# Kernel optimization log

Measured on AMD Instinct MI355X. Metric: run time of the kernel, lower is better.

Reference implementation:

```python
import jax, jax.numpy as jnp
import numpy as np

INPUT_SIZE = 500
SENTENCE_SIZE = 128


def setup_inputs() -> dict:
    key = jax.random.key(0)
    ks = jax.random.split(key, 20)
    B, D = 16, 512
    Ho, Hi, Hu = 4, 4, 4
    dh_ori = D // Ho          # 128
    dh = D // (Hi + Hu)       # 64
    s = 0.05
    code = jax.random.normal(ks[0], (B, INPUT_SIZE, D), jnp.float32)
    # binary sentence-membership mask (which code tokens belong to each sentence)
    input_sentence = (jax.random.uniform(ks[1], (B, SENTENCE_SIZE, INPUT_SIZE)) < 0.2).astype(jnp.float32)

    def W(k, h, dout):
        return jax.random.normal(k, (h, D, dout), jnp.float32) * s

    def b(k, h, dout):
        return jax.random.normal(k, (h, dout), jnp.float32) * 0.01

    return dict(
        code=code, input_sentence=input_sentence,
        Wq_ori=W(ks[2], Ho, dh_ori), bq_ori=b(ks[3], Ho, dh_ori),
        Wk_ori=W(ks[4], Ho, dh_ori), bk_ori=b(ks[5], Ho, dh_ori),
        Wq_in=W(ks[6], Hi, dh), bq_in=b(ks[7], Hi, dh),
        Wk_in=W(ks[8], Hi, dh), bk_in=b(ks[9], Hi, dh),
        Wv_in=W(ks[10], Hi, dh), bv_in=b(ks[11], Hi, dh),
        Wq_out=W(ks[12], Hu, dh), bq_out=b(ks[13], Hu, dh),
        Wk_out=W(ks[14], Hu, dh), bk_out=b(ks[15], Hu, dh),
        Wv_out=W(ks[16], Hu, dh), bv_out=b(ks[17], Hu, dh),
    )


def _proj(x, W, b):
    # x: (B, N, D), W: (H, D, F), b: (H, F) -> (B, H, N, F), relu Dense per head
    return jax.nn.relu(jnp.einsum('bnd,hdf->bhnf', x, W) + b[:, None, :])


def reference(code, input_sentence,
              Wq_ori, bq_ori, Wk_ori, bk_ori,
              Wq_in, bq_in, Wk_in, bk_in, Wv_in, bv_in,
              Wq_out, bq_out, Wk_out, bk_out, Wv_out, bv_out):
    B, S = input_sentence.shape[0], input_sentence.shape[1]
    sent = input_sentence

    # ---- original (ori) branch: max over heads of raw QK^T, mask, matmul code ----
    q = _proj(code, Wq_ori, bq_ori)
    k = _proj(code, Wk_ori, bk_ori)
    scores_ori = jnp.einsum('bhnf,bhmf->bhnm', q, k).max(axis=1)      # (B, N, N)
    sA = jnp.einsum('bsn,bnm->bsm', sent, scores_ori)                 # (B, S, N)
    out_ori = jnp.einsum('bsm,bmd->bsd', sent * sA, code)             # (B, S, D)

    # ---- in-mask heads ----
    qi = _proj(code, Wq_in, bq_in)
    ki = _proj(code, Wk_in, bk_in)
    vi = _proj(code, Wv_in, bv_in)
    sc = jnp.einsum('bhnf,bhmf->bhnm', qi, ki)                        # (B, Hi, N, N)
    sAi = jnp.einsum('bsn,bhnm->bhsm', sent, sc)                      # (B, Hi, S, N)
    out_in = jnp.einsum('bhsm,bhmf->bhsf', sent[:, None] * sAi, vi)   # (B, Hi, S, F)

    # ---- out-mask heads ----
    qo = _proj(code, Wq_out, bq_out)
    ko = _proj(code, Wk_out, bk_out)
    vo = _proj(code, Wv_out, bv_out)
    sco = jnp.einsum('bhnf,bhmf->bhnm', qo, ko)
    sAo = jnp.einsum('bsn,bhnm->bhsm', sent, sco)
    masked = (sent - 1.0)[:, None] * sAo                              # (B, Hu, S, N)
    include = sent.sum(axis=2)[:, None, :, None]                      # (B, 1, S, 1)
    masked = masked / (INPUT_SIZE - include) * include
    out_out = jnp.einsum('bhsm,bhmf->bhsf', masked, vo)               # (B, Hu, S, F)

    # original returns a list [ori, in_0..in_Hi-1, out_0..out_Hu-1]; concat along features
    in_flat = jnp.transpose(out_in, (0, 2, 1, 3)).reshape(B, S, -1)
    out_flat = jnp.transpose(out_out, (0, 2, 1, 3)).reshape(B, S, -1)
    return jnp.concatenate([out_ori, in_flat, out_flat], axis=-1)
```

## Files before the change

kernel.cpp:

```cpp
#include <hip/hip_runtime.h>
#include <cfloat>

#define B_  16
#define N_  500
#define NP  512
#define S_  128
#define D_  512
#define FO  128
#define FI  64

typedef unsigned short u16;
typedef __attribute__((ext_vector_type(8))) short bf8;
typedef __attribute__((ext_vector_type(4))) float f4;

#define MFMA(a,b,c) __builtin_amdgcn_mfma_f32_16x16x32_bf16((a),(b),(c),0,0,0)

__device__ __forceinline__ u16 f2b(float x){
    union{float f;unsigned u;} v; v.f=x;
    unsigned r = v.u + 0x7fffu + ((v.u>>16)&1u);
    return (u16)(r>>16);
}
__device__ __forceinline__ float b2f(u16 x){
    union{unsigned u;float f;} v; v.u=((unsigned)x)<<16; return v.f;
}
__device__ __forceinline__ bf8 ldb8(const u16* p){ return *(const bf8*)p; }

__device__ __forceinline__ void gl2lds16(const u16* g, u16* lds){
    __builtin_amdgcn_global_load_lds(
        (const __attribute__((address_space(1))) unsigned int*)g,
        (__attribute__((address_space(3))) unsigned int*)lds, 16, 0, 0);
}
__device__ __forceinline__ void vdrain(){
    asm volatile("s_waitcnt vmcnt(0)" ::: "memory");
}

struct PWAll { const float* W[8]; u16* WT[8]; };
__global__ __launch_bounds__(256) void prep_all(const float* __restrict__ code,
                                                u16* __restrict__ codeB,
                                                u16* __restrict__ codeT,
                                                PWAll a)
{
    __shared__ float T[64][65];
    const int t = threadIdx.x;
    const int x = blockIdx.x;
    if (x < 1024){
        const int b  = x >> 6;
        const int m0 = ((x >> 3) & 7) * 64;
        const int d0 = (x & 7) * 64;
        #pragma unroll
        for (int i=0;i<16;++i){
            int idx = t + i*256; int rr = idx>>6, cc = idx&63;
            int m = m0+rr;
            T[rr][cc] = (m < N_) ? code[((size_t)b*N_+m)*D_ + d0+cc] : 0.f;
        }
        __syncthreads();
        #pragma unroll
        for (int i=0;i<16;++i){
            int idx=t+i*256; int rr=idx>>6, cc=idx&63; int m=m0+rr;
            if (m<N_) codeB[((size_t)b*N_+m)*D_ + d0+cc] = f2b(T[rr][cc]);
        }
        #pragma unroll
        for (int i=0;i<16;++i){
            int idx=t+i*256; int dd=idx>>6, mm=idx&63;
            codeT[((size_t)b*D_ + d0+dd)*NP + m0+mm] = f2b(T[mm][dd]);
        }
    } else {
        const int v    = x - 1024;
        const int h    = v / 80;
        const int rem  = v - h*80;
        const int slot = rem >> 3;
        const int d0   = (rem & 7) * 64;
        const int widx = slot<4 ? (slot>>1) : slot-2;
        const int ftile= slot<4 ? (slot&1)  : 0;
        const int F    = slot<4 ? 128 : 64;
        const float* W = a.W[widx];
        u16* WT        = a.WT[widx];
        const int f0 = ftile*64;
        #pragma unroll
        for (int i=0;i<16;++i){
            int idx=t+i*256; int rr=idx>>6, cc=idx&63;
            T[rr][cc] = W[((size_t)h*D_ + d0+rr)*F + f0+cc];
        }
        __syncthreads();
        #pragma unroll
        for (int i=0;i<16;++i){
            int idx=t+i*256; int ff=idx>>6, dd=idx&63;
            WT[((size_t)h*F + f0+ff)*D_ + d0+dd] = f2b(T[dd][ff]);
        }
    }
}

__global__ __launch_bounds__(256) void prep_sent_pad(const float* __restrict__ sent,
                                                     u16* __restrict__ sentB,
                                                     float* __restrict__ inc,
                                                     u16* a0, u16* a1, u16* a2, u16* a3)
{
    const int t = threadIdx.x;
    const int x = blockIdx.x;
    if (x < 1024){
        const int b  = x >> 6;
        const int s  = (x & 63)*2 + (t >> 7);
        const int tl = t & 127;
        const float* row = sent + ((size_t)b*S_+s)*N_;
        float4 v = make_float4(0.f,0.f,0.f,0.f);
        const int n = tl*4;
        if (n < N_) v = *(const float4*)(row+n);
        float sum = v.x+v.y+v.z+v.w;
        ushort4 o; o.x=f2b(v.x); o.y=f2b(v.y); o.z=f2b(v.z); o.w=f2b(v.w);
        *(ushort4*)&sentB[((size_t)b*S_+s)*NP + n] = o;
        #pragma unroll
        for (int off=32; off; off>>=1) sum += __shfl_down(sum, off);
        __shared__ float ls[4];
        if ((t&63)==0) ls[t>>6]=sum;
        __syncthreads();
        if (tl==0) inc[b*S_+s] = ls[(t>>7)*2] + ls[(t>>7)*2+1];
    } else {
        const int u  = x - 1024;
        u16* arr4[4] = {a0,a1,a2,a3};
        u16* base = arr4[u>>6] + (size_t)(u&63)*FI*NP;
        for (int idx=t; idx<FI*12; idx+=256){
            int f = idx/12, n = N_ + idx%12;
            base[(size_t)f*NP + n] = 0;
        }
    }
}

struct GemmOut { const float* bias[8]; u16* dst[8]; };
union ProjLDS {
    u16 ab[4][4096];
    u16 ot[16896];
};
__global__ __launch_bounds__(256) void proj_gemm(const u16* __restrict__ codeB,
                                                 const u16* __restrict__ WallT,
                                                 GemmOut go)
{
    __shared__ alignas(16) ProjLDS L;

    const int t = threadIdx.x;
    const int w = t>>6, l = t&63, lane16 = l&15, lq = l>>4;
    const int bid = blockIdx.x;
    const int xcd = bid & 7;
    const int g   = bid >> 3;
    const int rt  = xcd*8 + g/20;
    const int ct  = g - (g/20)*20;
    const int r0 = rt*128;
    const int c0 = ct*128;
    const int wr = (w>>1)*64, wc = (w&1)*64;
    const int srow = l>>2;

    f4 acc[4][4] = {};

    auto STAGE = [&](u16* Ad, u16* Bd, int k0){
        #pragma unroll
        for (int iss=0; iss<2; ++iss){
            const int rbase = w*32 + iss*16;
            const int R  = rbase + srow;
            const int cg = ((l&3) ^ ((R>>1)&3))*8;
            gl2lds16(codeB + (size_t)(r0+R)*D_ + k0 + cg, Ad + rbase*32);
            gl2lds16(WallT + (size_t)(c0+R)*D_ + k0 + cg, Bd + rbase*32);
        }
    };
    auto COMPUTE = [&](const u16* Ad, const u16* Bd){
        bf8 af[4], bfr[4];
        #pragma unroll
        for (int i=0;i<4;++i){
            const int Ra = wr + i*16 + lane16;
            const int Rb = wc + i*16 + lane16;
            af[i]  = *(const bf8*)&Ad[Ra*32 + ((lq ^ ((Ra>>1)&3))*8)];
            bfr[i] = *(const bf8*)&Bd[Rb*32 + ((lq ^ ((Rb>>1)&3))*8)];
        }
        #pragma unroll
        for (int i=0;i<4;++i)
            #pragma unroll
            for (int j=0;j<4;++j)
                acc[i][j] = MFMA(af[i], bfr[j], acc[i][j]);
    };

    STAGE(L.ab[0], L.ab[2], 0);
    #pragma unroll
    for (int k0=0; k0<D_; k0+=64){
        vdrain(); __syncthreads();
        if (k0+32 < D_) STAGE(L.ab[1], L.ab[3], k0+32);
        COMPUTE(L.ab[0], L.ab[2]);
        vdrain(); __syncthreads();
        if (k0+64 < D_) STAGE(L.ab[0], L.ab[2], k0+64);
        COMPUTE(L.ab[1], L.ab[3]);
    }

    const int ri = (ct<4) ? 0 : (ct<8) ? 1 : 2 + ((ct-8)>>1);
    const bool tr = (ri==2)||(ri==4)||(ri==5)||(ri==7);

    vdrain(); __syncthreads();

    #pragma unroll
    for (int j=0;j<4;++j){
        const int c = c0 + wc + j*16 + lane16;
        const int idx = (c < 1024) ? (c & 511) : ((c-1024) & 255);
        const float bv = go.bias[ri][idx];
        if (tr){
            #pragma unroll
            for (int i=0;i<4;++i){
                ushort4 o4;
                float x0=acc[i][j][0]+bv, x1=acc[i][j][1]+bv, x2=acc[i][j][2]+bv, x3=acc[i][j][3]+bv;
                o4.x=f2b(x0>0.f?x0:0.f); o4.y=f2b(x1>0.f?x1:0.f);
                o4.z=f2b(x2>0.f?x2:0.f); o4.w=f2b(x3>0.f?x3:0.f);
                *(ushort4*)&L.ot[(wc+j*16+lane16)*132 + wr+i*16+lq*4] = o4;
            }
        } else {
            #pragma unroll
            for (int i=0;i<4;++i)
                #pragma unroll
                for (int reg=0;reg<4;++reg){
                    float x = acc[i][j][reg] + bv;
                    L.ot[(wr+i*16+lq*4+reg)*132 + wc+j*16+lane16] = f2b(x>0.f?x:0.f);
                }
        }
    }
    __syncthreads();

    if (tr){
        const int c  = t>>1;
        const int cg = c0 + c;
        const int u  = cg - 1024;
        const int hfv = u & 255, h = hfv>>6, f2 = hfv & 63;
        u16* dbase = go.dst[ri];
        const int half = t & 1;
        #pragma unroll
        for (int k2=0;k2<16;++k2){
            const int r  = half*64 + k2*4;
            const int rb = r0 + r;
            if (rb < 8000){
                const int b = rb/500, n = rb - b*500;
                *(ushort4*)&dbase[((size_t)(b*4+h)*FI + f2)*NP + n] =
                    *(const ushort4*)&L.ot[c*132 + r];
            }
        }
    } else {
        const int r  = t>>1;
        const int rb = r0 + r;
        if (rb < 8000){
            const int b = rb/500, n = rb - b*500;
            const int half = t & 1;
            const int cg0 = c0 + half*64;
            int h, f2base, F2;
            if (cg0 < 1024){ const int hf0 = cg0 & 511; h = hf0>>7; f2base = hf0 & 127; F2 = 128; }
            else           { const int hf0 = (cg0-1024) & 255; h = hf0>>6; f2base = hf0 & 63; F2 = 64; }
            u16* dstp = go.dst[ri] + ((size_t)(b*4+h)*N_ + n)*F2 + f2base;
            #pragma unroll
            for (int k2=0;k2<16;++k2)
                *(ushort4*)&dstp[k2*4] = *(const ushort4*)&L.ot[r*132 + half*64 + k2*4];
        }
    }
}

__global__ __launch_bounds__(256) void ms_mfma(const u16* __restrict__ q,
                                               const u16* __restrict__ k,
                                               u16* __restrict__ maxscT)
{
    __shared__ alignas(16) u16 Qs[64][136];
    __shared__ alignas(16) u16 Ks[128][136];
    const int t=threadIdx.x, w=t>>6, l=t&63, lane16=l&15, lq=l>>4;
    const int b=blockIdx.x, n0=blockIdx.y*64, m0=blockIdx.z*128;
    const int wr=(w>>1)*32, wc=(w&1)*64;

    f4 best[2][4];
    #pragma unroll
    for(int rt=0;rt<2;++rt)
        #pragma unroll
        for(int ct=0;ct<4;++ct)
            #pragma unroll
            for(int i=0;i<4;++i) best[rt][ct][i] = -FLT_MAX;

    for (int h=0;h<4;++h){
        const u16* qh = q + (size_t)(b*4+h)*N_*FO;
        const u16* kh = k + (size_t)(b*4+h)*N_*FO;
        #pragma unroll
        for (int i=0;i<4;++i){
            const int e=t+i*256, row=e>>4, kc=(e&15)*8;
            int n=n0+row; if(n>N_-1)n=N_-1;
            *(bf8*)&Qs[row][kc] = ldb8(qh + (size_t)n*FO + kc);
        }
        #pragma unroll
        for (int i=0;i<8;++i){
            const int e=t+i*256, row=e>>4, kc=(e&15)*8;
            int m=m0+row; if(m>N_-1)m=N_-1;
            *(bf8*)&Ks[row][kc] = ldb8(kh + (size_t)m*FO + kc);
        }
        __syncthreads();
        f4 acc[2][4]={};
        #pragma unroll
        for (int kk=0;kk<FO;kk+=32){
            bf8 a0=*(const bf8*)&Qs[wr+lane16][kk+lq*8];
            bf8 a1=*(const bf8*)&Qs[wr+16+lane16][kk+lq*8];
            #pragma unroll
            for(int ct=0;ct<4;++ct){
                bf8 bb=*(const bf8*)&Ks[wc+ct*16+lane16][kk+lq*8];
                acc[0][ct]=MFMA(a0,bb,acc[0][ct]);
                acc[1][ct]=MFMA(a1,bb,acc[1][ct]);
            }
        }
        #pragma unroll
        for(int rt=0;rt<2;++rt)
            #pragma unroll
            for(int ct=0;ct<4;++ct)
                #pragma unroll
                for(int i=0;i<4;++i) best[rt][ct][i] = fmaxf(best[rt][ct][i], acc[rt][ct][i]);
        __syncthreads();
    }
    #pragma unroll
    for(int rt=0;rt<2;++rt)
        #pragma unroll
        for(int ct=0;ct<4;++ct){
            const int m  = m0+wc+ct*16+lane16;
            const int nb = n0+wr+rt*16+lq*4;
            ushort4 o; o.x=f2b(best[rt][ct][0]); o.y=f2b(best[rt][ct][1]);
            o.z=f2b(best[rt][ct][2]); o.w=f2b(best[rt][ct][3]);
            *(ushort4*)&maxscT[((size_t)b*NP+m)*NP + nb] = o;
        }
}

__global__ __launch_bounds__(512) void saoo(const u16* __restrict__ sentB,
                                            const u16* __restrict__ maxscT,
                                            const u16* __restrict__ codeT,
                                            float* __restrict__ out)
{
    __shared__ u16 sAmS[16][520];
    const int b=blockIdx.x, s0=blockIdx.y*16;
    const int t=threadIdx.x, w=t>>6, l=t&63, lane16=l&15, lq=l>>4;

    {
        const int m0 = w*64;
        const u16* ap = sentB + ((size_t)b*S_ + s0+lane16)*NP + lq*8;
        const u16* bp[4];
        #pragma unroll
        for(int ct=0;ct<4;++ct) bp[ct] = maxscT + ((size_t)b*NP + m0+ct*16+lane16)*NP + lq*8;
        f4 acc[4] = {};
        for (int k0=0;k0<NP;k0+=32){
            bf8 av=ldb8(ap+k0);
            #pragma unroll
            for(int ct=0;ct<4;++ct) acc[ct]=MFMA(av, ldb8(bp[ct]+k0), acc[ct]);
        }
        #pragma unroll
        for(int ct=0;ct<4;++ct){
            const int m = m0+ct*16+lane16;
            #pragma unroll
            for(int reg=0;reg<4;++reg){
                const int s = s0+lq*4+reg;
                const float sv = b2f(sentB[((size_t)b*S_+s)*NP+m]);
                sAmS[lq*4+reg][m] = (sv != 0.f) ? f2b(acc[ct][reg]*sv) : (u16)0;
            }
        }
    }
    __syncthreads();
    {
        const int d0 = w*64;
        const u16* bp[4];
        #pragma unroll
        for(int ct=0;ct<4;++ct) bp[ct] = codeT + ((size_t)b*D_ + d0+ct*16+lane16)*NP + lq*8;
        f4 acc[4] = {};
        for (int k0=0;k0<NP;k0+=32){
            bf8 av = *(const bf8*)&sAmS[lane16][k0+lq*8];
            #pragma unroll
            for(int ct=0;ct<4;++ct) acc[ct]=MFMA(av, ldb8(bp[ct]+k0), acc[ct]);
        }
        #pragma unroll
        for(int ct=0;ct<4;++ct){
            const int d = d0+ct*16+lane16;
            #pragma unroll
            for(int reg=0;reg<4;++reg){
                const int s = s0+lq*4+reg;
                out[((size_t)b*S_+s)*1024 + d] = acc[ct][reg];
            }
        }
    }
}

struct AttnArgs { const u16* qT[2]; const u16* kp[2]; const u16* vT[2]; };
__global__ __launch_bounds__(256) void attn_fused(AttnArgs a,
                                                  const u16* __restrict__ sentB,
                                                  const float* __restrict__ inc,
                                                  float* __restrict__ out)
{
    __shared__ float red[4][32][68];
    __shared__ u16 qsS[32][72];
    __shared__ u16 Pw[4][32][72];
    const int bh=blockIdx.x, b=bh>>2, h=bh&3, s0=blockIdx.y*32, br=blockIdx.z;
    const u16* qT = a.qT[br];
    const u16* kp = a.kp[br];
    const u16* vT = a.vT[br];
    const int t=threadIdx.x, w=t>>6, l=t&63, lane16=l&15, lq=l>>4;

    {
        const u16 *ap[2], *bp[4];
        #pragma unroll
        for(int rt=0;rt<2;++rt) ap[rt] = sentB + ((size_t)b*S_ + s0+rt*16+lane16)*NP + w*128 + lq*8;
        #pragma unroll
        for(int ct=0;ct<4;++ct) bp[ct] = qT + ((size_t)bh*FI + ct*16+lane16)*NP + w*128 + lq*8;
        f4 acc[2][4] = {};
        #pragma unroll
        for (int k0=0;k0<128;k0+=32){
            bf8 a0=ldb8(ap[0]+k0), a1=ldb8(ap[1]+k0);
            #pragma unroll
            for(int ct=0;ct<4;++ct){
                bf8 bb=ldb8(bp[ct]+k0);
                acc[0][ct]=MFMA(a0,bb,acc[0][ct]);
                acc[1][ct]=MFMA(a1,bb,acc[1][ct]);
            }
        }
        #pragma unroll
        for(int rt=0;rt<2;++rt)
            #pragma unroll
            for(int ct=0;ct<4;++ct)
                #pragma unroll
                for(int reg=0;reg<4;++reg)
                    red[w][rt*16+lq*4+reg][ct*16+lane16] = acc[rt][ct][reg];
    }
    __syncthreads();
    {
        const int s=t>>3, f0=(t&7)*8;
        #pragma unroll
        for (int j=0;j<8;++j){
            float v = red[0][s][f0+j]+red[1][s][f0+j]+red[2][s][f0+j]+red[3][s][f0+j];
            qsS[s][f0+j] = f2b(v);
        }
    }
    __syncthreads();

    f4 accO[2][4] = {};
    #pragma unroll
    for (int c=0;c<2;++c){
        const int m0 = w*64 + c*256;
        f4 p[2][4] = {};
        const u16* bp[4];
        #pragma unroll
        for(int ct=0;ct<4;++ct){
            int m=m0+ct*16+lane16; if(m>N_-1)m=N_-1;
            bp[ct] = kp + ((size_t)bh*N_+m)*FI + lq*8;
        }
        #pragma unroll
        for (int kk=0; kk<FI; kk+=32){
            bf8 a0 = *(const bf8*)&qsS[lane16][kk+lq*8];
            bf8 a1 = *(const bf8*)&qsS[16+lane16][kk+lq*8];
            #pragma unroll
            for(int ct=0;ct<4;++ct){
                bf8 bb=ldb8(bp[ct]+kk);
                p[0][ct]=MFMA(a0,bb,p[0][ct]);
                p[1][ct]=MFMA(a1,bb,p[1][ct]);
            }
        }
        #pragma unroll
        for(int rt=0;rt<2;++rt)
            #pragma unroll
            for(int ct=0;ct<4;++ct){
                const int m = m0+ct*16+lane16;
                #pragma unroll
                for(int reg=0;reg<4;++reg){
                    const int s = s0+rt*16+lq*4+reg;
                    const float sv = b2f(sentB[((size_t)b*S_+s)*NP+m]);
                    const float wgt = br ? ((m<N_)? sv-1.f : 0.f) : sv;
                    Pw[w][rt*16+lq*4+reg][ct*16+lane16] = f2b(p[rt][ct][reg]*wgt);
                }
            }
        #pragma unroll
        for (int kk2=0; kk2<64; kk2+=32){
            bf8 a2[2];
            #pragma unroll
            for(int rt=0;rt<2;++rt) a2[rt] = *(const bf8*)&Pw[w][rt*16+lane16][kk2+lq*8];
            #pragma unroll
            for(int ct=0;ct<4;++ct){
                bf8 vv = ldb8(vT + ((size_t)bh*FI + ct*16+lane16)*NP + m0+kk2+lq*8);
                accO[0][ct]=MFMA(a2[0],vv,accO[0][ct]);
                accO[1][ct]=MFMA(a2[1],vv,accO[1][ct]);
            }
        }
    }
    #pragma unroll
    for(int rt=0;rt<2;++rt)
        #pragma unroll
        for(int ct=0;ct<4;++ct)
            #pragma unroll
            for(int reg=0;reg<4;++reg)
                red[w][rt*16+lq*4+reg][ct*16+lane16] = accO[rt][ct][reg];
    __syncthreads();
    {
        const int s=t>>3, f0=(t&7)*8;
        float fac = 1.f;
        if (br){ const float ic = inc[b*S_+s0+s]; fac = ic/(500.f-ic); }
        const size_t o = ((size_t)b*S_+s0+s)*1024 + (br?768:512) + h*FI + f0;
        #pragma unroll
        for (int j=0;j<8;++j){
            float v = red[0][s][f0+j]+red[1][s][f0+j]+red[2][s][f0+j]+red[3][s][f0+j];
            out[o+j] = v*fac;
        }
    }
}

extern "C" void kernel_launch(void* const* d_in, const int* in_sizes, int n_in,
                              void* d_out, int out_size, void* d_ws, size_t ws_size,
                              hipStream_t stream)
{
    const float* code   = (const float*)d_in[0];
    const float* sent   = (const float*)d_in[1];
    const float* Wq_ori = (const float*)d_in[2];
    const float* bq_ori = (const float*)d_in[3];
    const float* Wk_ori = (const float*)d_in[4];
    const float* bk_ori = (const float*)d_in[5];
    const float* Wq_in  = (const float*)d_in[6];
    const float* bq_in  = (const float*)d_in[7];
    const float* Wk_in  = (const float*)d_in[8];
    const float* bk_in  = (const float*)d_in[9];
    const float* Wv_in  = (const float*)d_in[10];
    const float* bv_in  = (const float*)d_in[11];
    const float* Wq_out = (const float*)d_in[12];
    const float* bq_out = (const float*)d_in[13];
    const float* Wk_out = (const float*)d_in[14];
    const float* bk_out = (const float*)d_in[15];
    const float* Wv_out = (const float*)d_in[16];
    const float* bv_out = (const float*)d_in[17];
    float* out = (float*)d_out;

    char* w = (char*)d_ws;
    u16*   codeB  = (u16*)(w);
    u16*   WallT  = (u16*)(w + 8388608);
    u16*   WTqo   = WallT;
    u16*   WTko   = WallT +  262144;
    u16*   WTqi   = WallT +  524288;
    u16*   WTki   = WallT +  655360;
    u16*   WTvi   = WallT +  786432;
    u16*   WTqu   = WallT +  917504;
    u16*   WTku   = WallT + 1048576;
    u16*   WTvu   = WallT + 1179648;
    u16*   sentB  = (u16*)(w + 11010048);
    float* incp   = (float*)(w + 13107200);
    u16* q_ori  = (u16*)(w + 13115392);
    u16* k_ori  = (u16*)(w + 21307392);
    u16* maxscT = (u16*)(w + 29499392);
    u16* codeT  = (u16*)(w + 37888000);
    u16* k_in   = (u16*)(w + 46276608);
    u16* k_out  = (u16*)(w + 50372608);
    u16* qT_in  = (u16*)(w + 54468608);
    u16* qT_out = (u16*)(w + 58662912);
    u16* vT_in  = (u16*)(w + 62857216);
    u16* vT_out = (u16*)(w + 67051520);

    PWAll pw;
    pw.W[0]=Wq_ori; pw.W[1]=Wk_ori; pw.W[2]=Wq_in; pw.W[3]=Wk_in;
    pw.W[4]=Wv_in;  pw.W[5]=Wq_out; pw.W[6]=Wk_out; pw.W[7]=Wv_out;
    pw.WT[0]=WTqo; pw.WT[1]=WTko; pw.WT[2]=WTqi; pw.WT[3]=WTki;
    pw.WT[4]=WTvi; pw.WT[5]=WTqu; pw.WT[6]=WTku; pw.WT[7]=WTvu;
    prep_all<<<dim3(1344), 256, 0, stream>>>(code, codeB, codeT, pw);
    prep_sent_pad<<<dim3(1280), 256, 0, stream>>>(sent, sentB, incp,
                                                  qT_in, qT_out, vT_in, vT_out);

    GemmOut go;
    go.bias[0]=bq_ori; go.bias[1]=bk_ori; go.bias[2]=bq_in; go.bias[3]=bk_in;
    go.bias[4]=bv_in;  go.bias[5]=bq_out; go.bias[6]=bk_out; go.bias[7]=bv_out;
    go.dst[0]=q_ori; go.dst[1]=k_ori; go.dst[2]=qT_in; go.dst[3]=k_in;
    go.dst[4]=vT_in; go.dst[5]=qT_out; go.dst[6]=k_out; go.dst[7]=vT_out;
    proj_gemm<<<dim3(1280), 256, 0, stream>>>(codeB, WallT, go);

    ms_mfma<<<dim3(16,8,4), 256, 0, stream>>>(q_ori, k_ori, maxscT);
    saoo<<<dim3(16,8), 512, 0, stream>>>(sentB, maxscT, codeT, out);

    AttnArgs aa;
    aa.qT[0]=qT_in;  aa.qT[1]=qT_out;
    aa.kp[0]=k_in;   aa.kp[1]=k_out;
    aa.vT[0]=vT_in;  aa.vT[1]=vT_out;
    attn_fused<<<dim3(64,4,2), 256, 0, stream>>>(aa, sentB, incp, out);
}
```

Measured before the change: 133.1 us.

## Merge prep kernels and co-schedule max-score with attention in one launch

```diff
diff --git a/kernel.cpp b/kernel.cpp
--- a/kernel.cpp
+++ b/kernel.cpp
@@ -35,10 +35,14 @@
 }
 
 struct PWAll { const float* W[8]; u16* WT[8]; };
-__global__ __launch_bounds__(256) void prep_all(const float* __restrict__ code,
-                                                u16* __restrict__ codeB,
-                                                u16* __restrict__ codeT,
-                                                PWAll a)
+__global__ __launch_bounds__(256) void prep_fused(const float* __restrict__ code,
+                                                  u16* __restrict__ codeB,
+                                                  u16* __restrict__ codeT,
+                                                  PWAll a,
+                                                  const float* __restrict__ sent,
+                                                  u16* __restrict__ sentB,
+                                                  float* __restrict__ inc,
+                                                  u16* a0, u16* a1, u16* a2, u16* a3)
 {
     __shared__ float T[64][65];
     const int t = threadIdx.x;
@@ -64,7 +68,7 @@
             int idx=t+i*256; int dd=idx>>6, mm=idx&63;
             codeT[((size_t)b*D_ + d0+dd)*NP + m0+mm] = f2b(T[mm][dd]);
         }
-    } else {
+    } else if (x < 1344){
         const int v    = x - 1024;
         const int h    = v / 80;
         const int rem  = v - h*80;
@@ -87,19 +91,10 @@
             int idx=t+i*256; int ff=idx>>6, dd=idx&63;
             WT[((size_t)h*F + f0+ff)*D_ + d0+dd] = f2b(T[dd][ff]);
         }
-    }
-}
-
-__global__ __launch_bounds__(256) void prep_sent_pad(const float* __restrict__ sent,
-                                                     u16* __restrict__ sentB,
-                                                     float* __restrict__ inc,
-                                                     u16* a0, u16* a1, u16* a2, u16* a3)
-{
-    const int t = threadIdx.x;
-    const int x = blockIdx.x;
-    if (x < 1024){
-        const int b  = x >> 6;
-        const int s  = (x & 63)*2 + (t >> 7);
+    } else if (x < 2368){
+        const int y  = x - 1344;
+        const int b  = y >> 6;
+        const int s  = (y & 63)*2 + (t >> 7);
         const int tl = t & 127;
         const float* row = sent + ((size_t)b*S_+s)*N_;
         float4 v = make_float4(0.f,0.f,0.f,0.f);
@@ -115,7 +110,7 @@
         __syncthreads();
         if (tl==0) inc[b*S_+s] = ls[(t>>7)*2] + ls[(t>>7)*2+1];
     } else {
-        const int u  = x - 1024;
+        const int u  = x - 2368;
         u16* arr4[4] = {a0,a1,a2,a3};
         u16* base = arr4[u>>6] + (size_t)(u&63)*FI*NP;
         for (int idx=t; idx<FI*12; idx+=256){
@@ -253,50 +248,170 @@
     }
 }
 
-__global__ __launch_bounds__(256) void ms_mfma(const u16* __restrict__ q,
-                                               const u16* __restrict__ k,
-                                               u16* __restrict__ maxscT)
+struct AttnArgs { const u16* qT[2]; const u16* kp[2]; const u16* vT[2]; };
+struct MsLDS  { u16 Qs[64][136]; u16 Ks[128][136]; };
+struct AtLDS  { float red[4][32][68]; u16 qsS[32][72]; u16 Pw[4][32][72]; };
+union MALDS   { MsLDS ms; AtLDS at; };
+
+__global__ __launch_bounds__(256) void msattn(const u16* __restrict__ q,
+                                              const u16* __restrict__ k,
+                                              u16* __restrict__ maxscT,
+                                              AttnArgs a,
+                                              const u16* __restrict__ sentB,
+                                              const float* __restrict__ inc,
+                                              float* __restrict__ out)
 {
-    __shared__ alignas(16) u16 Qs[64][136];
-    __shared__ alignas(16) u16 Ks[128][136];
+    __shared__ alignas(16) MALDS L;
     const int t=threadIdx.x, w=t>>6, l=t&63, lane16=l&15, lq=l>>4;
-    const int b=blockIdx.x, n0=blockIdx.y*64, m0=blockIdx.z*128;
-    const int wr=(w>>1)*32, wc=(w&1)*64;
-
-    f4 best[2][4];
-    #pragma unroll
-    for(int rt=0;rt<2;++rt)
-        #pragma unroll
-        for(int ct=0;ct<4;++ct)
-            #pragma unroll
-            for(int i=0;i<4;++i) best[rt][ct][i] = -FLT_MAX;
-
-    for (int h=0;h<4;++h){
-        const u16* qh = q + (size_t)(b*4+h)*N_*FO;
-        const u16* kh = k + (size_t)(b*4+h)*N_*FO;
-        #pragma unroll
-        for (int i=0;i<4;++i){
-            const int e=t+i*256, row=e>>4, kc=(e&15)*8;
-            int n=n0+row; if(n>N_-1)n=N_-1;
-            *(bf8*)&Qs[row][kc] = ldb8(qh + (size_t)n*FO + kc);
-        }
-        #pragma unroll
-        for (int i=0;i<8;++i){
-            const int e=t+i*256, row=e>>4, kc=(e&15)*8;
-            int m=m0+row; if(m>N_-1)m=N_-1;
-            *(bf8*)&Ks[row][kc] = ldb8(kh + (size_t)m*FO + kc);
+    const int idx = blockIdx.x >> 1;
+
+    if ((blockIdx.x & 1) == 0){
+        const int b=idx&15, n0=((idx>>4)&7)*64, m0=(idx>>7)*128;
+        const int wr=(w>>1)*32, wc=(w&1)*64;
+
+        f4 best[2][4];
+        #pragma unroll
+        for(int rt=0;rt<2;++rt)
+            #pragma unroll
+            for(int ct=0;ct<4;++ct)
+                #pragma unroll
+                for(int i=0;i<4;++i) best[rt][ct][i] = -FLT_MAX;
+
+        for (int h=0;h<4;++h){
+            const u16* qh = q + (size_t)(b*4+h)*N_*FO;
+            const u16* kh = k + (size_t)(b*4+h)*N_*FO;
+            #pragma unroll
+            for (int i=0;i<4;++i){
+                const int e=t+i*256, row=e>>4, kc=(e&15)*8;
+                int n=n0+row; if(n>N_-1)n=N_-1;
+                *(bf8*)&L.ms.Qs[row][kc] = ldb8(qh + (size_t)n*FO + kc);
+            }
+            #pragma unroll
+            for (int i=0;i<8;++i){
+                const int e=t+i*256, row=e>>4, kc=(e&15)*8;
+                int m=m0+row; if(m>N_-1)m=N_-1;
+                *(bf8*)&L.ms.Ks[row][kc] = ldb8(kh + (size_t)m*FO + kc);
+            }
+            __syncthreads();
+            f4 acc[2][4]={};
+            #pragma unroll
+            for (int kk=0;kk<FO;kk+=32){
+                bf8 a0=*(const bf8*)&L.ms.Qs[wr+lane16][kk+lq*8];
+                bf8 a1=*(const bf8*)&L.ms.Qs[wr+16+lane16][kk+lq*8];
+                #pragma unroll
+                for(int ct=0;ct<4;++ct){
+                    bf8 bb=*(const bf8*)&L.ms.Ks[wc+ct*16+lane16][kk+lq*8];
+                    acc[0][ct]=MFMA(a0,bb,acc[0][ct]);
+                    acc[1][ct]=MFMA(a1,bb,acc[1][ct]);
+                }
+            }
+            #pragma unroll
+            for(int rt=0;rt<2;++rt)
+                #pragma unroll
+                for(int ct=0;ct<4;++ct)
+                    #pragma unroll
+                    for(int i=0;i<4;++i) best[rt][ct][i] = fmaxf(best[rt][ct][i], acc[rt][ct][i]);
+            __syncthreads();
+        }
+        #pragma unroll
+        for(int rt=0;rt<2;++rt)
+            #pragma unroll
+            for(int ct=0;ct<4;++ct){
+                const int m  = m0+wc+ct*16+lane16;
+                const int nb = n0+wr+rt*16+lq*4;
+                ushort4 o; o.x=f2b(best[rt][ct][0]); o.y=f2b(best[rt][ct][1]);
+                o.z=f2b(best[rt][ct][2]); o.w=f2b(best[rt][ct][3]);
+                *(ushort4*)&maxscT[((size_t)b*NP+m)*NP + nb] = o;
+            }
+    } else {
+        const int bh=idx&63, b=bh>>2, h=bh&3, s0=((idx>>6)&3)*32, br=idx>>8;
+        const u16* qT = a.qT[br];
+        const u16* kp = a.kp[br];
+        const u16* vT = a.vT[br];
+
+        {
+            const u16 *ap[2], *bp[4];
+            #pragma unroll
+            for(int rt=0;rt<2;++rt) ap[rt] = sentB + ((size_t)b*S_ + s0+rt*16+lane16)*NP + w*128 + lq*8;
+            #pragma unroll
+            for(int ct=0;ct<4;++ct) bp[ct] = qT + ((size_t)bh*FI + ct*16+lane16)*NP + w*128 + lq*8;
+            f4 acc[2][4] = {};
+            #pragma unroll
+            for (int k0=0;k0<128;k0+=32){
+                bf8 a0=ldb8(ap[0]+k0), a1=ldb8(ap[1]+k0);
+                #pragma unroll
+                for(int ct=0;ct<4;++ct){
+                    bf8 bb=ldb8(bp[ct]+k0);
+                    acc[0][ct]=MFMA(a0,bb,acc[0][ct]);
+                    acc[1][ct]=MFMA(a1,bb,acc[1][ct]);
+                }
+            }
+            #pragma unroll
+            for(int rt=0;rt<2;++rt)
+                #pragma unroll
+                for(int ct=0;ct<4;++ct)
+                    #pragma unroll
+                    for(int reg=0;reg<4;++reg)
+                        L.at.red[w][rt*16+lq*4+reg][ct*16+lane16] = acc[rt][ct][reg];
         }
         __syncthreads();
-        f4 acc[2][4]={};
-        #pragma unroll
-        for (int kk=0;kk<FO;kk+=32){
-            bf8 a0=*(const bf8*)&Qs[wr+lane16][kk+lq*8];
-            bf8 a1=*(const bf8*)&Qs[wr+16+lane16][kk+lq*8];
+        {
+            const int s=t>>3, f0=(t&7)*8;
+            #pragma unroll
+            for (int j=0;j<8;++j){
+                float v = L.at.red[0][s][f0+j]+L.at.red[1][s][f0+j]
+                        + L.at.red[2][s][f0+j]+L.at.red[3][s][f0+j];
+                L.at.qsS[s][f0+j] = f2b(v);
+            }
+        }
+        __syncthreads();
+
+        f4 accO[2][4] = {};
+        #pragma unroll
+        for (int c=0;c<2;++c){
+            const int m0 = w*64 + c*256;
+            f4 p[2][4] = {};
+            const u16* bp[4];
             #pragma unroll
             for(int ct=0;ct<4;++ct){
-                bf8 bb=*(const bf8*)&Ks[wc+ct*16+lane16][kk+lq*8];
-                acc[0][ct]=MFMA(a0,bb,acc[0][ct]);
-                acc[1][ct]=MFMA(a1,bb,acc[1][ct]);
+                int m=m0+ct*16+lane16; if(m>N_-1)m=N_-1;
+                bp[ct] = kp + ((size_t)bh*N_+m)*FI + lq*8;
+            }
+            #pragma unroll
+            for (int kk=0; kk<FI; kk+=32){
+                bf8 a0 = *(const bf8*)&L.at.qsS[lane16][kk+lq*8];
+                bf8 a1 = *(const bf8*)&L.at.qsS[16+lane16][kk+lq*8];
+                #pragma unroll
+                for(int ct=0;ct<4;++ct){
+                    bf8 bb=ldb8(bp[ct]+kk);
+                    p[0][ct]=MFMA(a0,bb,p[0][ct]);
+                    p[1][ct]=MFMA(a1,bb,p[1][ct]);
+                }
+            }
+            #pragma unroll
+            for(int rt=0;rt<2;++rt)
+                #pragma unroll
+                for(int ct=0;ct<4;++ct){
+                    const int m = m0+ct*16+lane16;
+                    #pragma unroll
+                    for(int reg=0;reg<4;++reg){
+                        const int s = s0+rt*16+lq*4+reg;
+                        const float sv = b2f(sentB[((size_t)b*S_+s)*NP+m]);
+                        const float wgt = br ? ((m<N_)? sv-1.f : 0.f) : sv;
+                        L.at.Pw[w][rt*16+lq*4+reg][ct*16+lane16] = f2b(p[rt][ct][reg]*wgt);
+                    }
+                }
+            #pragma unroll
+            for (int kk2=0; kk2<64; kk2+=32){
+                bf8 a2[2];
+                #pragma unroll
+                for(int rt=0;rt<2;++rt) a2[rt] = *(const bf8*)&L.at.Pw[w][rt*16+lane16][kk2+lq*8];
+                #pragma unroll
+                for(int ct=0;ct<4;++ct){
+                    bf8 vv = ldb8(vT + ((size_t)bh*FI + ct*16+lane16)*NP + m0+kk2+lq*8);
+                    accO[0][ct]=MFMA(a2[0],vv,accO[0][ct]);
+                    accO[1][ct]=MFMA(a2[1],vv,accO[1][ct]);
+                }
             }
         }
         #pragma unroll
@@ -304,19 +419,22 @@
             #pragma unroll
             for(int ct=0;ct<4;++ct)
                 #pragma unroll
-                for(int i=0;i<4;++i) best[rt][ct][i] = fmaxf(best[rt][ct][i], acc[rt][ct][i]);
+                for(int reg=0;reg<4;++reg)
+                    L.at.red[w][rt*16+lq*4+reg][ct*16+lane16] = accO[rt][ct][reg];
         __syncthreads();
-    }
-    #pragma unroll
-    for(int rt=0;rt<2;++rt)
-        #pragma unroll
-        for(int ct=0;ct<4;++ct){
-            const int m  = m0+wc+ct*16+lane16;
-            const int nb = n0+wr+rt*16+lq*4;
-            ushort4 o; o.x=f2b(best[rt][ct][0]); o.y=f2b(best[rt][ct][1]);
-            o.z=f2b(best[rt][ct][2]); o.w=f2b(best[rt][ct][3]);
-            *(ushort4*)&maxscT[((size_t)b*NP+m)*NP + nb] = o;
-        }
+        {
+            const int s=t>>3, f0=(t&7)*8;
+            float fac = 1.f;
+            if (br){ const float ic = inc[b*S_+s0+s]; fac = ic/(500.f-ic); }
+            const size_t o = ((size_t)b*S_+s0+s)*1024 + (br?768:512) + h*FI + f0;
+            #pragma unroll
+            for (int j=0;j<8;++j){
+                float v = L.at.red[0][s][f0+j]+L.at.red[1][s][f0+j]
+                        + L.at.red[2][s][f0+j]+L.at.red[3][s][f0+j];
+                out[o+j] = v*fac;
+            }
+        }
+    }
 }
 
 __global__ __launch_bounds__(512) void saoo(const u16* __restrict__ sentB,
@@ -371,126 +489,6 @@
                 const int s = s0+lq*4+reg;
                 out[((size_t)b*S_+s)*1024 + d] = acc[ct][reg];
             }
-        }
-    }
-}
-
-struct AttnArgs { const u16* qT[2]; const u16* kp[2]; const u16* vT[2]; };
-__global__ __launch_bounds__(256) void attn_fused(AttnArgs a,
-                                                  const u16* __restrict__ sentB,
-                                                  const float* __restrict__ inc,
-                                                  float* __restrict__ out)
-{
-    __shared__ float red[4][32][68];
-    __shared__ u16 qsS[32][72];
-    __shared__ u16 Pw[4][32][72];
-    const int bh=blockIdx.x, b=bh>>2, h=bh&3, s0=blockIdx.y*32, br=blockIdx.z;
-    const u16* qT = a.qT[br];
-    const u16* kp = a.kp[br];
-    const u16* vT = a.vT[br];
-    const int t=threadIdx.x, w=t>>6, l=t&63, lane16=l&15, lq=l>>4;
-
-    {
-        const u16 *ap[2], *bp[4];
-        #pragma unroll
-        for(int rt=0;rt<2;++rt) ap[rt] = sentB + ((size_t)b*S_ + s0+rt*16+lane16)*NP + w*128 + lq*8;
-        #pragma unroll
-        for(int ct=0;ct<4;++ct) bp[ct] = qT + ((size_t)bh*FI + ct*16+lane16)*NP + w*128 + lq*8;
-        f4 acc[2][4] = {};
-        #pragma unroll
-        for (int k0=0;k0<128;k0+=32){
-            bf8 a0=ldb8(ap[0]+k0), a1=ldb8(ap[1]+k0);
-            #pragma unroll
-            for(int ct=0;ct<4;++ct){
-                bf8 bb=ldb8(bp[ct]+k0);
-                acc[0][ct]=MFMA(a0,bb,acc[0][ct]);
-                acc[1][ct]=MFMA(a1,bb,acc[1][ct]);
-            }
-        }
-        #pragma unroll
-        for(int rt=0;rt<2;++rt)
-            #pragma unroll
-            for(int ct=0;ct<4;++ct)
-                #pragma unroll
-                for(int reg=0;reg<4;++reg)
-                    red[w][rt*16+lq*4+reg][ct*16+lane16] = acc[rt][ct][reg];
-    }
-    __syncthreads();
-    {
-        const int s=t>>3, f0=(t&7)*8;
-        #pragma unroll
-        for (int j=0;j<8;++j){
-            float v = red[0][s][f0+j]+red[1][s][f0+j]+red[2][s][f0+j]+red[3][s][f0+j];
-            qsS[s][f0+j] = f2b(v);
-        }
-    }
-    __syncthreads();
-
-    f4 accO[2][4] = {};
-    #pragma unroll
-    for (int c=0;c<2;++c){
-        const int m0 = w*64 + c*256;
-        f4 p[2][4] = {};
-        const u16* bp[4];
-        #pragma unroll
-        for(int ct=0;ct<4;++ct){
-            int m=m0+ct*16+lane16; if(m>N_-1)m=N_-1;
-            bp[ct] = kp + ((size_t)bh*N_+m)*FI + lq*8;
-        }
-        #pragma unroll
-        for (int kk=0; kk<FI; kk+=32){
-            bf8 a0 = *(const bf8*)&qsS[lane16][kk+lq*8];
-            bf8 a1 = *(const bf8*)&qsS[16+lane16][kk+lq*8];
-            #pragma unroll
-            for(int ct=0;ct<4;++ct){
-                bf8 bb=ldb8(bp[ct]+kk);
-                p[0][ct]=MFMA(a0,bb,p[0][ct]);
-                p[1][ct]=MFMA(a1,bb,p[1][ct]);
-            }
-        }
-        #pragma unroll
-        for(int rt=0;rt<2;++rt)
-            #pragma unroll
-            for(int ct=0;ct<4;++ct){
-                const int m = m0+ct*16+lane16;
-                #pragma unroll
-                for(int reg=0;reg<4;++reg){
-                    const int s = s0+rt*16+lq*4+reg;
-                    const float sv = b2f(sentB[((size_t)b*S_+s)*NP+m]);
-                    const float wgt = br ? ((m<N_)? sv-1.f : 0.f) : sv;
-                    Pw[w][rt*16+lq*4+reg][ct*16+lane16] = f2b(p[rt][ct][reg]*wgt);
-                }
-            }
-        #pragma unroll
-        for (int kk2=0; kk2<64; kk2+=32){
-            bf8 a2[2];
-            #pragma unroll
-            for(int rt=0;rt<2;++rt) a2[rt] = *(const bf8*)&Pw[w][rt*16+lane16][kk2+lq*8];
-            #pragma unroll
-            for(int ct=0;ct<4;++ct){
-                bf8 vv = ldb8(vT + ((size_t)bh*FI + ct*16+lane16)*NP + m0+kk2+lq*8);
-                accO[0][ct]=MFMA(a2[0],vv,accO[0][ct]);
-                accO[1][ct]=MFMA(a2[1],vv,accO[1][ct]);
-            }
-        }
-    }
-    #pragma unroll
-    for(int rt=0;rt<2;++rt)
-        #pragma unroll
-        for(int ct=0;ct<4;++ct)
-            #pragma unroll
-            for(int reg=0;reg<4;++reg)
-                red[w][rt*16+lq*4+reg][ct*16+lane16] = accO[rt][ct][reg];
-    __syncthreads();
-    {
-        const int s=t>>3, f0=(t&7)*8;
-        float fac = 1.f;
-        if (br){ const float ic = inc[b*S_+s0+s]; fac = ic/(500.f-ic); }
-        const size_t o = ((size_t)b*S_+s0+s)*1024 + (br?768:512) + h*FI + f0;
-        #pragma unroll
-        for (int j=0;j<8;++j){
-            float v = red[0][s][f0+j]+red[1][s][f0+j]+red[2][s][f0+j]+red[3][s][f0+j];
-            out[o+j] = v*fac;
         }
     }
 }
@@ -548,9 +546,9 @@
     pw.W[4]=Wv_in;  pw.W[5]=Wq_out; pw.W[6]=Wk_out; pw.W[7]=Wv_out;
     pw.WT[0]=WTqo; pw.WT[1]=WTko; pw.WT[2]=WTqi; pw.WT[3]=WTki;
     pw.WT[4]=WTvi; pw.WT[5]=WTqu; pw.WT[6]=WTku; pw.WT[7]=WTvu;
-    prep_all<<<dim3(1344), 256, 0, stream>>>(code, codeB, codeT, pw);
-    prep_sent_pad<<<dim3(1280), 256, 0, stream>>>(sent, sentB, incp,
-                                                  qT_in, qT_out, vT_in, vT_out);
+    prep_fused<<<dim3(2624), 256, 0, stream>>>(code, codeB, codeT, pw,
+                                               sent, sentB, incp,
+                                               qT_in, qT_out, vT_in, vT_out);
 
     GemmOut go;
     go.bias[0]=bq_ori; go.bias[1]=bk_ori; go.bias[2]=bq_in; go.bias[3]=bk_in;
@@ -559,12 +557,11 @@
     go.dst[4]=vT_in; go.dst[5]=qT_out; go.dst[6]=k_out; go.dst[7]=vT_out;
     proj_gemm<<<dim3(1280), 256, 0, stream>>>(codeB, WallT, go);
 
-    ms_mfma<<<dim3(16,8,4), 256, 0, stream>>>(q_ori, k_ori, maxscT);
-    saoo<<<dim3(16,8), 512, 0, stream>>>(sentB, maxscT, codeT, out);
-
     AttnArgs aa;
     aa.qT[0]=qT_in;  aa.qT[1]=qT_out;
     aa.kp[0]=k_in;   aa.kp[1]=k_out;
     aa.vT[0]=vT_in;  aa.vT[1]=vT_out;
-    attn_fused<<<dim3(64,4,2), 256, 0, stream>>>(aa, sentB, incp, out);
-}
+    msattn<<<dim3(1024), 256, 0, stream>>>(q_ori, k_ori, maxscT, aa, sentB, incp, out);
+
+    saoo<<<dim3(16,8), 512, 0, stream>>>(sentB, maxscT, codeT, out);
+}
```

New measurement: 128.8 us. -3.3%, faster.
